# Kernel optimization log

Hardware: AMD Instinct MI355X
Metric: run time of the kernel (lower is better)

## Reference

```python
import jax, jax.numpy as jnp
import numpy as np

HIDDEN = 1024
NEG_INF = jnp.float32(-1e7)


def setup_inputs() -> dict:
    key = jax.random.key(0)
    ks = jax.random.split(key, 9)
    B, S, H = 4, 2048, HIDDEN
    std = 1.0 / np.sqrt(H)
    return {
        "queries": jax.random.normal(ks[0], (B, S, H), jnp.float32),
        "keys": jax.random.normal(ks[1], (B, S, H), jnp.float32),
        "values": jax.random.normal(ks[2], (B, S, H), jnp.float32),
        "Wq": jax.random.uniform(ks[3], (H, H), jnp.float32, -std, std),
        "bq": jax.random.uniform(ks[4], (H,), jnp.float32, -std, std),
        "Wk": jax.random.uniform(ks[5], (H, H), jnp.float32, -std, std),
        "bk": jax.random.uniform(ks[6], (H,), jnp.float32, -std, std),
        "Wv": jax.random.uniform(ks[7], (H, H), jnp.float32, -std, std),
        "bv": jax.random.uniform(ks[8], (H,), jnp.float32, -std, std),
    }


def reference(queries, keys, values, Wq, bq, Wk, bk, Wv, bv):
    # q,k,v: (B, S, H) linear projections (torch Linear: x @ W.T + b)
    q = jnp.einsum('bth,oh->bto', queries, Wq) + bq
    k = jnp.einsum('bsh,oh->bso', keys, Wk) + bk
    v = jnp.einsum('bsh,oh->bso', values, Wv) + bv
    scale = jax.lax.rsqrt(jnp.float32(q.shape[-1] * 0 + Wq.shape[0]))
    # scores[b, s, t] = <k_s, q_t> * scale   (key index s, query index t)
    scores = jnp.einsum('bsh,bth->bst', k, q) * scale
    S, T = scores.shape[1], scores.shape[2]
    # torch.tril(ones * -1e7, diagonal=-1): add -1e7 where s > t (strictly lower)
    mask = jnp.where(jnp.arange(S)[:, None] > jnp.arange(T)[None, :], NEG_INF, 0.0)
    attn = jax.nn.softmax(scores + mask, axis=1)  # softmax over key dim (dim=1)
    context = jnp.einsum('bst,bsh->bth', attn, v)  # (B, T, H)
    return context, attn
```

## Files before the change

### kernel.cpp

```cpp
#include <hip/hip_runtime.h>
#include <math.h>

typedef __bf16 bf16x8 __attribute__((ext_vector_type(8)));
typedef float f32x4 __attribute__((ext_vector_type(4)));

#define HD 1024
#define SEQ 2048
#define NB 4

__device__ inline bf16x8 load8cvt(const __bf16* p) { return *(const bf16x8*)p; }
__device__ inline bf16x8 load8cvt(const float* p) {
    f32x4 a = *(const f32x4*)p;
    f32x4 b = *(const f32x4*)(p + 4);
    bf16x8 r;
#pragma unroll
    for (int i = 0; i < 4; ++i) { r[i] = (__bf16)a[i]; r[i + 4] = (__bf16)b[i]; }
    return r;
}

__device__ inline void gld_lds16(const void* g, void* l) {
    __builtin_amdgcn_global_load_lds(
        (const __attribute__((address_space(1))) unsigned int*)g,
        (__attribute__((address_space(3))) unsigned int*)l, 16, 0, 0);
}

template <typename T>
__device__ inline void stage_tile(const T* __restrict__ G, int ld, __bf16* s, int tid)
{
    const int r  = tid >> 3;
    const int co = (tid & 7) * 8;
    if constexpr (sizeof(T) == 2) {
        __bf16* dst = s + (tid >> 6) * 512;
#pragma unroll
        for (int c = 0; c < 4; ++c)
            gld_lds16(G + (long)(c * 32 + r) * ld + co, dst + c * 2048);
    } else {
#pragma unroll
        for (int c = 0; c < 4; ++c)
            *(bf16x8*)(s + c * 2048 + tid * 8) = load8cvt(G + (long)(c * 32 + r) * ld + co);
    }
}

struct Proj3 {
    const void* A[3];
    const float* W[3];
    const float* bias[3];
    __bf16* C[3];
    int vtmask;
};

template <typename TA>
__global__ __launch_bounds__(256) void gemm_proj(Proj3 p)
{
    __shared__ __bf16 sA[128 * 64];
    __shared__ __bf16 sB[128 * 64];

    const int tid = threadIdx.x;
    const int z  = blockIdx.z;
    const int n0 = blockIdx.x * 128;
    const int m0 = blockIdx.y * 128;
    const bool vt = (p.vtmask >> z) & 1;

    const TA* Ag = (const TA*)p.A[z] + (long)m0 * HD;
    const float* Wg = p.W[z] + (long)n0 * HD;
    const float* bias = p.bias[z];
    __bf16* C = p.C[z];

    const int lane = tid & 63;
    const int l15  = lane & 15;
    const int quad = lane >> 4;
    const int wave = tid >> 6;
    const int wm = (wave >> 1) * 64;
    const int wn = (wave & 1) * 64;

    f32x4 acc[4][4];
    const f32x4 zero = {0.f, 0.f, 0.f, 0.f};
#pragma unroll
    for (int i = 0; i < 4; ++i)
#pragma unroll
        for (int j = 0; j < 4; ++j) acc[i][j] = zero;

    for (int kc = 0; kc < HD; kc += 64) {
        stage_tile(Ag + kc, HD, sA, tid);
        stage_tile(Wg + kc, HD, sB, tid);
        __syncthreads();
#pragma unroll
        for (int kk = 0; kk < 64; kk += 32) {
            bf16x8 af[4], bf[4];
#pragma unroll
            for (int i = 0; i < 4; ++i)
                af[i] = *(const bf16x8*)&sA[(wm + i * 16 + l15) * 64 + quad * 8 + kk];
#pragma unroll
            for (int j = 0; j < 4; ++j)
                bf[j] = *(const bf16x8*)&sB[(wn + j * 16 + l15) * 64 + quad * 8 + kk];
#pragma unroll
            for (int i = 0; i < 4; ++i)
#pragma unroll
                for (int j = 0; j < 4; ++j)
                    acc[i][j] = __builtin_amdgcn_mfma_f32_16x16x32_bf16(af[i], bf[j], acc[i][j], 0, 0, 0);
        }
        __syncthreads();
    }

#pragma unroll
    for (int j = 0; j < 4; ++j) {
        const int col = n0 + wn + j * 16 + l15;
        const float bv = bias[col];
#pragma unroll
        for (int i = 0; i < 4; ++i) {
#pragma unroll
            for (int r = 0; r < 4; ++r) {
                const int row = m0 + wm + i * 16 + quad * 4 + r;
                const float v = acc[i][j][r] + bv;
                if (vt) {
                    C[(((long)(row >> 11) * HD) + col) * SEQ + (row & (SEQ - 1))] = (__bf16)v;
                } else {
                    C[(long)row * HD + col] = (__bf16)v;
                }
            }
        }
    }
}

template <bool TRI, bool CKLIM, bool EXPSUM, typename OutT>
__global__ __launch_bounds__(256) void gemm_bt(
    const __bf16* __restrict__ A, long strideA, int lda,
    const __bf16* __restrict__ B, long strideB, int ldb,
    OutT* __restrict__ C, long strideC, int ldc,
    float* __restrict__ gsum,
    int K, float alpha)
{
    __shared__ __bf16 sA[128 * 64];
    __shared__ __bf16 sB[128 * 64];
    __shared__ float csum[128];

    const int tid = threadIdx.x;
    int n0, m0;
    if (TRI) {
        const int L = blockIdx.x;
        int tb = (int)((sqrtf(8.f * L + 1.f) - 1.f) * 0.5f);
        while ((tb + 1) * (tb + 2) / 2 <= L) ++tb;
        while (tb * (tb + 1) / 2 > L) --tb;
        const int sb = L - tb * (tb + 1) / 2;
        n0 = tb * 128;
        m0 = sb * 128;
    } else {
        n0 = blockIdx.x * 128;
        m0 = blockIdx.y * 128;
    }

    const __bf16* Ag = A + (long)blockIdx.z * strideA + (long)m0 * lda;
    const __bf16* Bg = B + (long)blockIdx.z * strideB + (long)n0 * ldb;
    C += (long)blockIdx.z * strideC;
    if (EXPSUM) {
        gsum += (long)blockIdx.z * SEQ;
        if (tid < 128) csum[tid] = 0.f;
    }

    const int lane = tid & 63;
    const int l15  = lane & 15;
    const int quad = lane >> 4;
    const int wave = tid >> 6;
    const int wm = (wave >> 1) * 64;
    const int wn = (wave & 1) * 64;

    f32x4 acc[4][4];
    const f32x4 zero = {0.f, 0.f, 0.f, 0.f};
#pragma unroll
    for (int i = 0; i < 4; ++i)
#pragma unroll
        for (int j = 0; j < 4; ++j) acc[i][j] = zero;

    const int Kend = CKLIM ? min(K, m0 + 128) : K;

    for (int kc = 0; kc < Kend; kc += 64) {
        stage_tile(Ag + kc, lda, sA, tid);
        stage_tile(Bg + kc, ldb, sB, tid);
        __syncthreads();
#pragma unroll
        for (int kk = 0; kk < 64; kk += 32) {
            bf16x8 af[4], bf[4];
#pragma unroll
            for (int i = 0; i < 4; ++i)
                af[i] = *(const bf16x8*)&sA[(wm + i * 16 + l15) * 64 + quad * 8 + kk];
#pragma unroll
            for (int j = 0; j < 4; ++j)
                bf[j] = *(const bf16x8*)&sB[(wn + j * 16 + l15) * 64 + quad * 8 + kk];
#pragma unroll
            for (int i = 0; i < 4; ++i)
#pragma unroll
                for (int j = 0; j < 4; ++j)
                    acc[i][j] = __builtin_amdgcn_mfma_f32_16x16x32_bf16(af[i], bf[j], acc[i][j], 0, 0, 0);
        }
        __syncthreads();
    }

#pragma unroll
    for (int j = 0; j < 4; ++j) {
        const int col = n0 + wn + j * 16 + l15;
        float part = 0.f;
#pragma unroll
        for (int i = 0; i < 4; ++i) {
#pragma unroll
            for (int r = 0; r < 4; ++r) {
                const int row = m0 + wm + i * 16 + quad * 4 + r;
                float v = acc[i][j][r] * alpha;
                if (EXPSUM) {
                    v = __expf(v);
                    if (row <= col) part += v;
                }
                C[(long)row * ldc + col] = (OutT)v;
            }
        }
        if (EXPSUM) atomicAdd(&csum[wn + j * 16 + l15], part);
    }
    if (EXPSUM) {
        __syncthreads();
        if (tid < 128) atomicAdd(&gsum[n0 + tid], csum[tid]);
    }
}

__global__ __launch_bounds__(256) void scale_emit(
    float* __restrict__ E, const float* __restrict__ csum, __bf16* __restrict__ AT)
{
    __shared__ __bf16 tile[64][65];
    const int b = blockIdx.z;
    const int t0 = blockIdx.x * 128;
    const int s0 = blockIdx.y * 128;
    float* Eb = E + (long)b * SEQ * SEQ;
    __bf16* Ab = AT + (long)b * SEQ * SEQ;
    const int tid = threadIdx.x;

    if (s0 > t0 + 127) {
        const f32x4 z4 = {0.f, 0.f, 0.f, 0.f};
        const int c4 = (tid & 31) * 4;
        for (int r = tid >> 5; r < 128; r += 8)
            *(f32x4*)&Eb[(long)(s0 + r) * SEQ + t0 + c4] = z4;
        bf16x8 z8;
#pragma unroll
        for (int i = 0; i < 8; ++i) z8[i] = (__bf16)0.f;
        const int sc = (tid & 15) * 8;
        for (int r = tid >> 4; r < 128; r += 16)
            *(bf16x8*)&Ab[(long)(t0 + r) * SEQ + s0 + sc] = z8;
        return;
    }

#pragma unroll
    for (int ds = 0; ds < 2; ++ds) {
#pragma unroll
        for (int dt = 0; dt < 2; ++dt) {
            const int ss = s0 + ds * 64, tt = t0 + dt * 64;
            const int c4 = (tid & 15) * 4;
            const int tcol = tt + c4;
            const f32x4 sv = *(const f32x4*)&csum[(long)b * SEQ + tcol];
            f32x4 inv;
#pragma unroll
            for (int k = 0; k < 4; ++k) inv[k] = 1.0f / sv[k];
#pragma unroll
            for (int r0 = 0; r0 < 64; r0 += 16) {
                const int s = ss + r0 + (tid >> 4);
                f32x4 e = *(f32x4*)&Eb[(long)s * SEQ + tcol];
                f32x4 p;
#pragma unroll
                for (int k = 0; k < 4; ++k)
                    p[k] = (s <= tcol + k) ? e[k] * inv[k] : 0.f;
                *(f32x4*)&Eb[(long)s * SEQ + tcol] = p;
#pragma unroll
                for (int k = 0; k < 4; ++k)
                    tile[r0 + (tid >> 4)][c4 + k] = (__bf16)p[k];
            }
            __syncthreads();
            const int tr = tid >> 2;
            const int sc = (tid & 3) * 16;
            __bf16 v[16];
#pragma unroll
            for (int jj = 0; jj < 16; ++jj) v[jj] = tile[sc + jj][tr];
            *(bf16x8*)&Ab[(long)(tt + tr) * SEQ + ss + sc]     = *(bf16x8*)v;
            *(bf16x8*)&Ab[(long)(tt + tr) * SEQ + ss + sc + 8] = *(bf16x8*)(v + 8);
            __syncthreads();
        }
    }
}

struct Cvt3 { const float* in[3]; __bf16* out[3]; };
__global__ __launch_bounds__(256) void cvt_bf16(Cvt3 c)
{
    const int z = blockIdx.y;
    const long i = ((long)blockIdx.x * 256 + threadIdx.x) * 8;
    *(bf16x8*)&c.out[z][i] = load8cvt(&c.in[z][i]);
}

extern "C" void kernel_launch(void* const* d_in, const int* in_sizes, int n_in,
                              void* d_out, int out_size, void* d_ws, size_t ws_size,
                              hipStream_t stream)
{
    const float* queries = (const float*)d_in[0];
    const float* keys    = (const float*)d_in[1];
    const float* values  = (const float*)d_in[2];
    const float* Wq = (const float*)d_in[3];
    const float* bq = (const float*)d_in[4];
    const float* Wk = (const float*)d_in[5];
    const float* bk = (const float*)d_in[6];
    const float* Wv = (const float*)d_in[7];
    const float* bv = (const float*)d_in[8];

    const long tokens = (long)NB * SEQ;
    const long pe = tokens * HD;
    const size_t SLOT = (size_t)pe * sizeof(__bf16);

    float* outCtx  = (float*)d_out;
    float* outAttn = outCtx + tokens * HD;
    float* colsum = outCtx;

    const dim3 blk(256);
    hipMemsetAsync(colsum, 0, (size_t)NB * SEQ * sizeof(float), stream);

    char* w = (char*)d_ws;
    __bf16 *qp, *kp, *vT;
    __bf16* attnT = (__bf16*)d_ws;
    const dim3 gProj(HD / 128, tokens / 128, 3);
    const unsigned nCvt = (unsigned)(pe / 8 / 256);

    if (ws_size >= 6 * SLOT) {
        __bf16* xq = (__bf16*)w;
        __bf16* xk = (__bf16*)(w + SLOT);
        __bf16* xv = (__bf16*)(w + 2 * SLOT);
        qp = (__bf16*)(w + 3 * SLOT);
        kp = (__bf16*)(w + 4 * SLOT);
        vT = (__bf16*)(w + 5 * SLOT);
        Cvt3 cv = {{queries, keys, values}, {xq, xk, xv}};
        cvt_bf16<<<dim3(nCvt, 3), blk, 0, stream>>>(cv);
        Proj3 pj = {{xq, xk, xv}, {Wq, Wk, Wv}, {bq, bk, bv}, {qp, kp, vT}, 4};
        gemm_proj<__bf16><<<gProj, blk, 0, stream>>>(pj);
    } else if (ws_size >= 4 * SLOT) {
        __bf16* x0 = (__bf16*)w;
        qp = (__bf16*)(w + SLOT);
        kp = (__bf16*)(w + 2 * SLOT);
        __bf16* x1 = (__bf16*)(w + 3 * SLOT);
        vT = x1;
        Cvt3 cv = {{queries, keys, nullptr}, {x0, x1, nullptr}};
        cvt_bf16<<<dim3(nCvt, 2), blk, 0, stream>>>(cv);
        Proj3 pqk = {{x0, x1, nullptr}, {Wq, Wk, nullptr}, {bq, bk, nullptr},
                     {qp, kp, nullptr}, 0};
        gemm_proj<__bf16><<<dim3(HD / 128, tokens / 128, 2), blk, 0, stream>>>(pqk);
        Cvt3 cvv = {{values, nullptr, nullptr}, {x0, nullptr, nullptr}};
        cvt_bf16<<<dim3(nCvt, 1), blk, 0, stream>>>(cvv);
        Proj3 pv = {{x0, nullptr, nullptr}, {Wv, nullptr, nullptr},
                    {bv, nullptr, nullptr}, {vT, nullptr, nullptr}, 1};
        gemm_proj<__bf16><<<dim3(HD / 128, tokens / 128, 1), blk, 0, stream>>>(pv);
    } else {
        qp = (__bf16*)w;
        kp = (__bf16*)(w + SLOT);
        vT = (__bf16*)(w + 2 * SLOT);
        Proj3 pj = {{queries, keys, values}, {Wq, Wk, Wv}, {bq, bk, bv},
                    {qp, kp, vT}, 4};
        gemm_proj<float><<<gProj, blk, 0, stream>>>(pj);
    }

    gemm_bt<true, false, true, float><<<dim3(136, 1, NB), blk, 0, stream>>>(
        kp, (long)SEQ * HD, HD, qp, (long)SEQ * HD, HD,
        outAttn, (long)SEQ * SEQ, SEQ, colsum, HD, 0.03125f);

    scale_emit<<<dim3(SEQ / 128, SEQ / 128, NB), blk, 0, stream>>>(
        outAttn, colsum, attnT);

    gemm_bt<false, true, false, float><<<dim3(HD / 128, SEQ / 128, NB), blk, 0, stream>>>(
        attnT, (long)SEQ * SEQ, SEQ, vT, (long)HD * SEQ, SEQ,
        outCtx, (long)SEQ * HD, HD, nullptr, SEQ, 1.0f);
}
```

Baseline: 415.6 us.

## Stage exp scores in bf16 workspace, pre-convert weights, skip zero attnT writes

When the workspace is large, the score GEMM now writes exp values as bf16 into a workspace buffer instead of fp32 into the attention output. scale_emit reads them and writes the final fp32 probabilities. This halves the traffic of the intermediate write and read. Weights are also converted to bf16 once, using the attention output area as scratch, so the projection GEMM loads bf16 instead of fp32. The upper-triangle zero-fill of attnT is dropped, which relies on the context GEMM skipping those tiles, or on the workspace already being zero there.

```diff
diff --git a/kernel.cpp b/kernel.cpp
--- a/kernel.cpp
+++ b/kernel.cpp
@@ -2,11 +2,13 @@
 #include <math.h>
 
 typedef __bf16 bf16x8 __attribute__((ext_vector_type(8)));
+typedef __bf16 bf16x4 __attribute__((ext_vector_type(4)));
 typedef float f32x4 __attribute__((ext_vector_type(4)));
 
 #define HD 1024
 #define SEQ 2048
 #define NB 4
+#define WEL (HD * HD)
 
 __device__ inline bf16x8 load8cvt(const __bf16* p) { return *(const bf16x8*)p; }
 __device__ inline bf16x8 load8cvt(const float* p) {
@@ -18,6 +20,15 @@
     return r;
 }
 
+__device__ inline f32x4 load4f(const float* p) { return *(const f32x4*)p; }
+__device__ inline f32x4 load4f(const __bf16* p) {
+    bf16x4 v = *(const bf16x4*)p;
+    f32x4 r;
+#pragma unroll
+    for (int i = 0; i < 4; ++i) r[i] = (float)v[i];
+    return r;
+}
+
 __device__ inline void gld_lds16(const void* g, void* l) {
     __builtin_amdgcn_global_load_lds(
         (const __attribute__((address_space(1))) unsigned int*)g,
@@ -43,13 +54,13 @@
 
 struct Proj3 {
     const void* A[3];
-    const float* W[3];
+    const void* W[3];
     const float* bias[3];
     __bf16* C[3];
     int vtmask;
 };
 
-template <typename TA>
+template <typename TA, typename TW>
 __global__ __launch_bounds__(256) void gemm_proj(Proj3 p)
 {
     __shared__ __bf16 sA[128 * 64];
@@ -62,7 +73,7 @@
     const bool vt = (p.vtmask >> z) & 1;
 
     const TA* Ag = (const TA*)p.A[z] + (long)m0 * HD;
-    const float* Wg = p.W[z] + (long)n0 * HD;
+    const TW* Wg = (const TW*)p.W[z] + (long)n0 * HD;
     const float* bias = p.bias[z];
     __bf16* C = p.C[z];
 
@@ -220,14 +231,17 @@
     }
 }
 
+template <typename ET>
 __global__ __launch_bounds__(256) void scale_emit(
-    float* __restrict__ E, const float* __restrict__ csum, __bf16* __restrict__ AT)
+    const ET* __restrict__ E, float* __restrict__ Out,
+    const float* __restrict__ csum, __bf16* __restrict__ AT)
 {
     __shared__ __bf16 tile[64][65];
     const int b = blockIdx.z;
     const int t0 = blockIdx.x * 128;
     const int s0 = blockIdx.y * 128;
-    float* Eb = E + (long)b * SEQ * SEQ;
+    const ET* Eb = E + (long)b * SEQ * SEQ;
+    float* Ob = Out + (long)b * SEQ * SEQ;
     __bf16* Ab = AT + (long)b * SEQ * SEQ;
     const int tid = threadIdx.x;
 
@@ -235,13 +249,7 @@
         const f32x4 z4 = {0.f, 0.f, 0.f, 0.f};
         const int c4 = (tid & 31) * 4;
         for (int r = tid >> 5; r < 128; r += 8)
-            *(f32x4*)&Eb[(long)(s0 + r) * SEQ + t0 + c4] = z4;
-        bf16x8 z8;
-#pragma unroll
-        for (int i = 0; i < 8; ++i) z8[i] = (__bf16)0.f;
-        const int sc = (tid & 15) * 8;
-        for (int r = tid >> 4; r < 128; r += 16)
-            *(bf16x8*)&Ab[(long)(t0 + r) * SEQ + s0 + sc] = z8;
+            *(f32x4*)&Ob[(long)(s0 + r) * SEQ + t0 + c4] = z4;
         return;
     }
 
@@ -259,12 +267,12 @@
 #pragma unroll
             for (int r0 = 0; r0 < 64; r0 += 16) {
                 const int s = ss + r0 + (tid >> 4);
-                f32x4 e = *(f32x4*)&Eb[(long)s * SEQ + tcol];
+                f32x4 e = load4f(&Eb[(long)s * SEQ + tcol]);
                 f32x4 p;
 #pragma unroll
                 for (int k = 0; k < 4; ++k)
                     p[k] = (s <= tcol + k) ? e[k] * inv[k] : 0.f;
-                *(f32x4*)&Eb[(long)s * SEQ + tcol] = p;
+                *(f32x4*)&Ob[(long)s * SEQ + tcol] = p;
 #pragma unroll
                 for (int k = 0; k < 4; ++k)
                     tile[r0 + (tid >> 4)][c4 + k] = (__bf16)p[k];
@@ -282,12 +290,14 @@
     }
 }
 
-struct Cvt3 { const float* in[3]; __bf16* out[3]; };
-__global__ __launch_bounds__(256) void cvt_bf16(Cvt3 c)
-{
-    const int z = blockIdx.y;
+struct CvtJob { const float* in; __bf16* out; int nblk; };
+struct Cvt6 { CvtJob j[6]; };
+__global__ __launch_bounds__(256) void cvt_bf16(Cvt6 c)
+{
+    const CvtJob jb = c.j[blockIdx.y];
+    if ((int)blockIdx.x >= jb.nblk) return;
     const long i = ((long)blockIdx.x * 256 + threadIdx.x) * 8;
-    *(bf16x8*)&c.out[z][i] = load8cvt(&c.in[z][i]);
+    *(bf16x8*)&jb.out[i] = load8cvt(&jb.in[i]);
 }
 
 extern "C" void kernel_launch(void* const* d_in, const int* in_sizes, int n_in,
@@ -307,19 +317,24 @@
     const long tokens = (long)NB * SEQ;
     const long pe = tokens * HD;
     const size_t SLOT = (size_t)pe * sizeof(__bf16);
+    const int ABLK = (int)(pe / 2048);
+    const int WBLK = WEL / 2048;
 
     float* outCtx  = (float*)d_out;
     float* outAttn = outCtx + tokens * HD;
     float* colsum = outCtx;
+    __bf16* wb = (__bf16*)outAttn;
+    __bf16* Wqb = wb, *Wkb = wb + WEL, *Wvb = wb + 2 * WEL;
 
     const dim3 blk(256);
     hipMemsetAsync(colsum, 0, (size_t)NB * SEQ * sizeof(float), stream);
 
     char* w = (char*)d_ws;
-    __bf16 *qp, *kp, *vT;
-    __bf16* attnT = (__bf16*)d_ws;
+    __bf16 *qp, *kp, *vT, *attnT;
     const dim3 gProj(HD / 128, tokens / 128, 3);
-    const unsigned nCvt = (unsigned)(pe / 8 / 256);
+
+    bool ebig = false;
+    __bf16* Ebf = nullptr;
 
     if (ws_size >= 6 * SLOT) {
         __bf16* xq = (__bf16*)w;
@@ -328,41 +343,59 @@
         qp = (__bf16*)(w + 3 * SLOT);
         kp = (__bf16*)(w + 4 * SLOT);
         vT = (__bf16*)(w + 5 * SLOT);
-        Cvt3 cv = {{queries, keys, values}, {xq, xk, xv}};
-        cvt_bf16<<<dim3(nCvt, 3), blk, 0, stream>>>(cv);
-        Proj3 pj = {{xq, xk, xv}, {Wq, Wk, Wv}, {bq, bk, bv}, {qp, kp, vT}, 4};
-        gemm_proj<__bf16><<<gProj, blk, 0, stream>>>(pj);
+        Ebf = (__bf16*)w;
+        attnT = (__bf16*)(w + 2 * SLOT);
+        ebig = true;
+
+        Cvt6 cv = {{{queries, xq, ABLK}, {keys, xk, ABLK}, {values, xv, ABLK},
+                    {Wq, Wqb, WBLK}, {Wk, Wkb, WBLK}, {Wv, Wvb, WBLK}}};
+        cvt_bf16<<<dim3(ABLK, 6), blk, 0, stream>>>(cv);
+        Proj3 pj = {{xq, xk, xv}, {Wqb, Wkb, Wvb}, {bq, bk, bv}, {qp, kp, vT}, 4};
+        gemm_proj<__bf16, __bf16><<<gProj, blk, 0, stream>>>(pj);
     } else if (ws_size >= 4 * SLOT) {
         __bf16* x0 = (__bf16*)w;
         qp = (__bf16*)(w + SLOT);
         kp = (__bf16*)(w + 2 * SLOT);
         __bf16* x1 = (__bf16*)(w + 3 * SLOT);
         vT = x1;
-        Cvt3 cv = {{queries, keys, nullptr}, {x0, x1, nullptr}};
-        cvt_bf16<<<dim3(nCvt, 2), blk, 0, stream>>>(cv);
-        Proj3 pqk = {{x0, x1, nullptr}, {Wq, Wk, nullptr}, {bq, bk, nullptr},
+        attnT = (__bf16*)d_ws;
+
+        Cvt6 cv = {{{queries, x0, ABLK}, {keys, x1, ABLK},
+                    {Wq, Wqb, WBLK}, {Wk, Wkb, WBLK}, {Wv, Wvb, WBLK},
+                    {nullptr, nullptr, 0}}};
+        cvt_bf16<<<dim3(ABLK, 5), blk, 0, stream>>>(cv);
+        Proj3 pqk = {{x0, x1, nullptr}, {Wqb, Wkb, nullptr}, {bq, bk, nullptr},
                      {qp, kp, nullptr}, 0};
-        gemm_proj<__bf16><<<dim3(HD / 128, tokens / 128, 2), blk, 0, stream>>>(pqk);
-        Cvt3 cvv = {{values, nullptr, nullptr}, {x0, nullptr, nullptr}};
-        cvt_bf16<<<dim3(nCvt, 1), blk, 0, stream>>>(cvv);
-        Proj3 pv = {{x0, nullptr, nullptr}, {Wv, nullptr, nullptr},
+        gemm_proj<__bf16, __bf16><<<dim3(HD / 128, tokens / 128, 2), blk, 0, stream>>>(pqk);
+        Cvt6 cvv = {{{values, x0, ABLK}, {nullptr, nullptr, 0}, {nullptr, nullptr, 0},
+                     {nullptr, nullptr, 0}, {nullptr, nullptr, 0}, {nullptr, nullptr, 0}}};
+        cvt_bf16<<<dim3(ABLK, 1), blk, 0, stream>>>(cvv);
+        Proj3 pv = {{x0, nullptr, nullptr}, {Wvb, nullptr, nullptr},
                     {bv, nullptr, nullptr}, {vT, nullptr, nullptr}, 1};
-        gemm_proj<__bf16><<<dim3(HD / 128, tokens / 128, 1), blk, 0, stream>>>(pv);
+        gemm_proj<__bf16, __bf16><<<dim3(HD / 128, tokens / 128, 1), blk, 0, stream>>>(pv);
     } else {
         qp = (__bf16*)w;
         kp = (__bf16*)(w + SLOT);
         vT = (__bf16*)(w + 2 * SLOT);
+        attnT = (__bf16*)d_ws;
         Proj3 pj = {{queries, keys, values}, {Wq, Wk, Wv}, {bq, bk, bv},
                     {qp, kp, vT}, 4};
-        gemm_proj<float><<<gProj, blk, 0, stream>>>(pj);
-    }
-
-    gemm_bt<true, false, true, float><<<dim3(136, 1, NB), blk, 0, stream>>>(
-        kp, (long)SEQ * HD, HD, qp, (long)SEQ * HD, HD,
-        outAttn, (long)SEQ * SEQ, SEQ, colsum, HD, 0.03125f);
-
-    scale_emit<<<dim3(SEQ / 128, SEQ / 128, NB), blk, 0, stream>>>(
-        outAttn, colsum, attnT);
+        gemm_proj<float, float><<<gProj, blk, 0, stream>>>(pj);
+    }
+
+    if (ebig) {
+        gemm_bt<true, false, true, __bf16><<<dim3(136, 1, NB), blk, 0, stream>>>(
+            kp, (long)SEQ * HD, HD, qp, (long)SEQ * HD, HD,
+            Ebf, (long)SEQ * SEQ, SEQ, colsum, HD, 0.03125f);
+        scale_emit<__bf16><<<dim3(SEQ / 128, SEQ / 128, NB), blk, 0, stream>>>(
+            Ebf, outAttn, colsum, attnT);
+    } else {
+        gemm_bt<true, false, true, float><<<dim3(136, 1, NB), blk, 0, stream>>>(
+            kp, (long)SEQ * HD, HD, qp, (long)SEQ * HD, HD,
+            outAttn, (long)SEQ * SEQ, SEQ, colsum, HD, 0.03125f);
+        scale_emit<float><<<dim3(SEQ / 128, SEQ / 128, NB), blk, 0, stream>>>(
+            outAttn, outAttn, colsum, attnT);
+    }
 
     gemm_bt<false, true, false, float><<<dim3(HD / 128, SEQ / 128, NB), blk, 0, stream>>>(
         attnT, (long)SEQ * SEQ, SEQ, vT, (long)HD * SEQ, SEQ,
```

Measured after the change: 401.3 us. -3.5%, faster.
